# Performance work log

Measured on AMD Instinct MI355X. Metric: run time of the kernel, lower is better.

The kernel has to match this reference:

```python
import jax, jax.numpy as jnp
import numpy as np

PH, PW = 7, 7          # output_size
GRID = 2               # sampling_ratio
SCALES = (0.25, 0.125, 0.0625, 0.03125)  # 2^round(log2(feat/img)) per level
LVL_MIN, LVL_MAX = 2, 5                  # -log2(scales[0]), -log2(scales[-1])
CANON_SCALE, CANON_LVL = 224.0, 4.0
EPS = 1e-6


def setup_inputs() -> dict:
    key = jax.random.key(0)
    ks = jax.random.split(key, 6)
    B, C = 2, 256
    sizes = [(200, 200), (100, 100), (50, 50), (25, 25)]
    inp = {f"feat{i}": jax.random.normal(ks[i], (B, C, h, w), jnp.float32)
           for i, (h, w) in enumerate(sizes)}
    Nb = 256
    # boxes in 800x800 image coords, x1y1 + positive wh so 0<=x1<x2, 0<=y1<y2
    xy = jax.random.uniform(ks[4], (B, Nb, 2), jnp.float32, 0.0, 700.0)
    wh = jax.random.uniform(ks[5], (B, Nb, 2), jnp.float32, 32.0, 512.0)
    inp["boxes"] = jnp.concatenate([xy, xy + wh], axis=-1)
    return inp


def _roi_align_level(feat, b_idx, rois, scale):
    """torchvision roi_align, aligned=False. feat [B,C,H,W], rois [R,4] -> [R,C,PH,PW]."""
    H, W = feat.shape[2], feat.shape[3]
    x1 = rois[:, 0] * scale
    y1 = rois[:, 1] * scale
    x2 = rois[:, 2] * scale
    y2 = rois[:, 3] * scale
    roi_w = jnp.maximum(x2 - x1, 1.0)
    roi_h = jnp.maximum(y2 - y1, 1.0)
    bin_w = roi_w / PW
    bin_h = roi_h / PH
    # sub-bin sampling offsets: (bin + (i+0.5)/grid) for each bin, flattened [PH*GRID]
    gy = (jnp.arange(PH, dtype=jnp.float32)[:, None]
          + (jnp.arange(GRID, dtype=jnp.float32)[None, :] + 0.5) / GRID).reshape(-1)
    gx = (jnp.arange(PW, dtype=jnp.float32)[:, None]
          + (jnp.arange(GRID, dtype=jnp.float32)[None, :] + 0.5) / GRID).reshape(-1)
    ys = y1[:, None] + gy[None, :] * bin_h[:, None]   # [R, PH*G]
    xs = x1[:, None] + gx[None, :] * bin_w[:, None]   # [R, PW*G]
    y = ys[:, :, None]                                 # [R, PH*G, 1]
    x = xs[:, None, :]                                 # [R, 1, PW*G]
    valid = (y >= -1.0) & (y <= H) & (x >= -1.0) & (x <= W)
    yc = jnp.clip(y, 0.0, H - 1)
    xc = jnp.clip(x, 0.0, W - 1)
    yl = jnp.floor(yc).astype(jnp.int32)
    xl = jnp.floor(xc).astype(jnp.int32)
    yh = jnp.minimum(yl + 1, H - 1)
    xh = jnp.minimum(xl + 1, W - 1)
    ly = yc - yl.astype(yc.dtype)
    lx = xc - xl.astype(xc.dtype)
    hy = 1.0 - ly
    hx = 1.0 - lx
    b = b_idx[:, None, None]

    def gather(yi, xi):
        # advanced indexing with slice in channel dim -> [R, PH*G, PW*G, C]
        return feat[b, :, yi, xi]

    val = ((hy * hx)[..., None] * gather(yl, xl)
           + (hy * lx)[..., None] * gather(yl, xh)
           + (ly * hx)[..., None] * gather(yh, xl)
           + (ly * lx)[..., None] * gather(yh, xh))
    val = jnp.where(valid[..., None], val, 0.0)
    R, C = rois.shape[0], feat.shape[1]
    # average over the GRIDxGRID sampling points of each bin
    val = val.reshape(R, PH, GRID, PW, GRID, C).mean(axis=(2, 4))  # [R,PH,PW,C]
    return jnp.transpose(val, (0, 3, 1, 2))                        # [R,C,PH,PW]


def reference(feat0, feat1, feat2, feat3, boxes):
    feats = [feat0, feat1, feat2, feat3]
    B, Nb = boxes.shape[0], boxes.shape[1]
    rois = boxes.reshape(-1, 4)                               # convert_to_roi_format
    b_idx = jnp.repeat(jnp.arange(B), Nb)
    # LevelMapper (FPN eq. 1)
    s = jnp.sqrt(jnp.maximum((rois[:, 2] - rois[:, 0]) * (rois[:, 3] - rois[:, 1]), 0.0))
    lvl = jnp.floor(CANON_LVL + jnp.log2(s / CANON_SCALE + EPS))
    lvl = jnp.clip(lvl, LVL_MIN, LVL_MAX).astype(jnp.int32) - LVL_MIN  # [R] in [0,3]
    out = jnp.zeros((rois.shape[0], feats[0].shape[1], PH, PW), feats[0].dtype)
    for l, (f, sc) in enumerate(zip(feats, SCALES)):
        pooled = _roi_align_level(f, b_idx, rois, sc)
        out = jnp.where((lvl == l)[:, None, None, None], pooled, out)
    return out
```

## Files before the change

kernel.cpp:

```cpp
#include <hip/hip_runtime.h>


#define PHW 49
#define NCHUNK 8
#define CH 32
#define NC 4
#define PSIZE 1024

__global__ __launch_bounds__(256) void msroi_kernel(
    const float* __restrict__ f0, const float* __restrict__ f1,
    const float* __restrict__ f2, const float* __restrict__ f3,
    const float* __restrict__ boxes, float* __restrict__ out)
{
    const int C = 256, Nb = 256;
    const int r = blockIdx.x;
    const int chunk = blockIdx.y;
    const int tid = threadIdx.x;
    const int b = r / Nb;

    const float x1b = boxes[r * 4 + 0];
    const float y1b = boxes[r * 4 + 1];
    const float x2b = boxes[r * 4 + 2];
    const float y2b = boxes[r * 4 + 3];
    const float area = fmaxf((x2b - x1b) * (y2b - y1b), 0.0f);
    const float s = sqrtf(area);
    float lv = floorf(4.0f + log2f(s / 224.0f + 1e-6f));
    lv = fminf(fmaxf(lv, 2.0f), 5.0f);
    const int lvl = (int)lv - 2;

    const float* feat;
    int H, W;
    float scale;
    switch (lvl) {
        case 0:  feat = f0; H = 200; W = 200; scale = 0.25f;    break;
        case 1:  feat = f1; H = 100; W = 100; scale = 0.125f;   break;
        case 2:  feat = f2; H = 50;  W = 50;  scale = 0.0625f;  break;
        default: feat = f3; H = 25;  W = 25;  scale = 0.03125f; break;
    }
    const int HW = H * W;

    const float x1 = x1b * scale, y1 = y1b * scale;
    const float x2 = x2b * scale, y2 = y2b * scale;
    const float roi_w = fmaxf(x2 - x1, 1.0f);
    const float roi_h = fmaxf(y2 - y1, 1.0f);
    const float bin_w = roi_w * (1.0f / 7.0f);
    const float bin_h = roi_h * (1.0f / 7.0f);

    const float ys0 = fminf(fmaxf(y1 + 0.25f * bin_h, 0.0f), (float)(H - 1));
    const float ys1 = fminf(fmaxf(y1 + 6.75f * bin_h, 0.0f), (float)(H - 1));
    const float xs0 = fminf(fmaxf(x1 + 0.25f * bin_w, 0.0f), (float)(W - 1));
    const float xs1 = fminf(fmaxf(x1 + 6.75f * bin_w, 0.0f), (float)(W - 1));
    const int row0 = (int)floorf(ys0);
    const int row1 = min((int)floorf(ys1) + 1, H - 1);
    const int col0 = (int)floorf(xs0);
    const int col1 = min((int)floorf(xs1) + 1, W - 1);
    const int prows = row1 - row0 + 1;
    const int pcols = col1 - col0 + 1;
    const int psize = prows * pcols;
    const int wstride = W - pcols;
    const float inv_pcols = 1.0f / (float)pcols;

    int goff[4];
#pragma unroll
    for (int k = 0; k < 4; ++k) {
        const int e = tid + k * 256;
        const int ec = min(e, psize - 1);
        const int rr = (int)floorf(((float)ec + 0.5f) * inv_pcols);
        goff[k] = ec + rr * wstride;
    }

    const int bin = tid & 63;
    const bool active = bin < PHW;
    int   offs[16];
    float wts[16];
    {
        const int bb = active ? bin : 0;
        const int ph = bb / 7;
        const int pw = bb - ph * 7;
#pragma unroll
        for (int g = 0; g < 4; ++g) {
            const int iy = g >> 1, ix = g & 1;
            const float gy = (float)ph + ((float)iy + 0.5f) * 0.5f;
            const float gx = (float)pw + ((float)ix + 0.5f) * 0.5f;
            const float y = y1 + gy * bin_h;
            const float x = x1 + gx * bin_w;
            const bool valid = (y >= -1.0f) && (y <= (float)H) &&
                               (x >= -1.0f) && (x <= (float)W);
            const float yc = fminf(fmaxf(y, 0.0f), (float)(H - 1));
            const float xc = fminf(fmaxf(x, 0.0f), (float)(W - 1));
            const int yl = (int)floorf(yc);
            const int xl = (int)floorf(xc);
            const int yh = min(yl + 1, H - 1);
            const int xh = min(xl + 1, W - 1);
            const float ly = yc - (float)yl;
            const float lx = xc - (float)xl;
            const float hy = 1.0f - ly, hx = 1.0f - lx;
            const float m = valid ? 0.25f : 0.0f;
            const int ry0 = (yl - row0) * pcols, ry1 = (yh - row0) * pcols;
            const int cx0 = xl - col0, cx1 = xh - col0;
            offs[g * 4 + 0] = ry0 + cx0;  wts[g * 4 + 0] = hy * hx * m;
            offs[g * 4 + 1] = ry0 + cx1;  wts[g * 4 + 1] = hy * lx * m;
            offs[g * 4 + 2] = ry1 + cx0;  wts[g * 4 + 2] = ly * hx * m;
            offs[g * 4 + 3] = ry1 + cx1;  wts[g * 4 + 3] = ly * lx * m;
        }
    }

    __shared__ float lds[NC * PSIZE];
    const int cslot = tid >> 6;
    const int cbase = chunk * CH;
    const float* __restrict__ fch =
        feat + (size_t)(b * C + cbase) * HW + (row0 * W + col0);
    const size_t outBase = (size_t)r * C * PHW + (size_t)cbase * PHW;

    for (int cc = 0; cc < CH; cc += NC) {
        float buf[NC][4];
#pragma unroll
        for (int ch = 0; ch < NC; ++ch) {
            const float* __restrict__ gp = fch + (size_t)(cc + ch) * HW;
#pragma unroll
            for (int k = 0; k < 4; ++k)
                buf[ch][k] = gp[goff[k]];
        }
#pragma unroll
        for (int ch = 0; ch < NC; ++ch) {
#pragma unroll
            for (int k = 0; k < 4; ++k)
                lds[ch * PSIZE + tid + k * 256] = buf[ch][k];
        }
        __syncthreads();

        if (active) {
            const float* __restrict__ p = &lds[cslot * PSIZE];
            float acc = 0.0f;
#pragma unroll
            for (int k = 0; k < 16; ++k)
                acc += wts[k] * p[offs[k]];
            out[outBase + (size_t)(cc + cslot) * PHW + bin] = acc;
        }
        __syncthreads();
    }
}

extern "C" void kernel_launch(void* const* d_in, const int* in_sizes, int n_in,
                              void* d_out, int out_size, void* d_ws, size_t ws_size,
                              hipStream_t stream) {
    const float* f0 = (const float*)d_in[0];
    const float* f1 = (const float*)d_in[1];
    const float* f2 = (const float*)d_in[2];
    const float* f3 = (const float*)d_in[3];
    const float* boxes = (const float*)d_in[4];
    float* out = (float*)d_out;

    const int R = in_sizes[4] / 4;
    dim3 grid(R, NCHUNK);
    msroi_kernel<<<grid, 256, 0, stream>>>(f0, f1, f2, f3, boxes, out);
}
```

Baseline: 180.6 us.

## Use single-wave blocks with channel-interleaved float4 LDS and register prefetch

```diff
diff --git a/kernel.cpp b/kernel.cpp
--- a/kernel.cpp
+++ b/kernel.cpp
@@ -4,10 +4,9 @@
 #define PHW 49
 #define NCHUNK 8
 #define CH 32
-#define NC 4
 #define PSIZE 1024
 
-__global__ __launch_bounds__(256) void msroi_kernel(
+__global__ __launch_bounds__(64) void msroi_kernel(
     const float* __restrict__ f0, const float* __restrict__ f1,
     const float* __restrict__ f2, const float* __restrict__ f3,
     const float* __restrict__ boxes, float* __restrict__ out)
@@ -60,16 +59,17 @@
     const int wstride = W - pcols;
     const float inv_pcols = 1.0f / (float)pcols;
 
-    int goff[4];
+    int goff[16];
 #pragma unroll
-    for (int k = 0; k < 4; ++k) {
-        const int e = tid + k * 256;
+    for (int k = 0; k < 16; ++k) {
+        const int e = tid + k * 64;
         const int ec = min(e, psize - 1);
         const int rr = (int)floorf(((float)ec + 0.5f) * inv_pcols);
         goff[k] = ec + rr * wstride;
     }
+    const int kmax = (psize + 63) >> 6;
 
-    const int bin = tid & 63;
+    const int bin = tid;
     const bool active = bin < PHW;
     int   offs[16];
     float wts[16];
@@ -105,40 +105,60 @@
         }
     }
 
-    __shared__ float lds[NC * PSIZE];
-    const int cslot = tid >> 6;
+    __shared__ float4 lds4[PSIZE];
+
     const int cbase = chunk * CH;
     const float* __restrict__ fch =
         feat + (size_t)(b * C + cbase) * HW + (row0 * W + col0);
-    const size_t outBase = (size_t)r * C * PHW + (size_t)cbase * PHW;
+    float* __restrict__ outp =
+        out + (size_t)r * C * PHW + (size_t)cbase * PHW + bin;
 
-    for (int cc = 0; cc < CH; cc += NC) {
-        float buf[NC][4];
+    float4 buf[16];
+
+#define LOADR(CCV)                                                         \
+    do {                                                                   \
+        const float* __restrict__ g0 = fch + (size_t)((CCV) + 0) * HW;     \
+        const float* __restrict__ g1 = fch + (size_t)((CCV) + 1) * HW;     \
+        const float* __restrict__ g2 = fch + (size_t)((CCV) + 2) * HW;     \
+        const float* __restrict__ g3 = fch + (size_t)((CCV) + 3) * HW;     \
+        _Pragma("unroll")                                                  \
+        for (int k = 0; k < 16; ++k) {                                     \
+            if (k < kmax) {       \
+                buf[k].x = g0[goff[k]];                                    \
+                buf[k].y = g1[goff[k]];                                    \
+                buf[k].z = g2[goff[k]];                                    \
+                buf[k].w = g3[goff[k]];                                    \
+            }                                                              \
+        }                                                                  \
+    } while (0)
+
+    LOADR(0);
+    for (int cc = 0; cc < CH; cc += 4) {
+        __syncthreads();
 #pragma unroll
-        for (int ch = 0; ch < NC; ++ch) {
-            const float* __restrict__ gp = fch + (size_t)(cc + ch) * HW;
-#pragma unroll
-            for (int k = 0; k < 4; ++k)
-                buf[ch][k] = gp[goff[k]];
-        }
-#pragma unroll
-        for (int ch = 0; ch < NC; ++ch) {
-#pragma unroll
-            for (int k = 0; k < 4; ++k)
-                lds[ch * PSIZE + tid + k * 256] = buf[ch][k];
-        }
+        for (int k = 0; k < 16; ++k)
+            if (k < kmax) lds4[tid + k * 64] = buf[k];
         __syncthreads();
 
+        if (cc + 4 < CH) LOADR(cc + 4);
+
         if (active) {
-            const float* __restrict__ p = &lds[cslot * PSIZE];
-            float acc = 0.0f;
+            float4 acc = make_float4(0.0f, 0.0f, 0.0f, 0.0f);
 #pragma unroll
-            for (int k = 0; k < 16; ++k)
-                acc += wts[k] * p[offs[k]];
-            out[outBase + (size_t)(cc + cslot) * PHW + bin] = acc;
+            for (int j = 0; j < 16; ++j) {
+                const float4 v = lds4[offs[j]];
+                acc.x += wts[j] * v.x;
+                acc.y += wts[j] * v.y;
+                acc.z += wts[j] * v.z;
+                acc.w += wts[j] * v.w;
+            }
+            outp[(size_t)(cc + 0) * PHW] = acc.x;
+            outp[(size_t)(cc + 1) * PHW] = acc.y;
+            outp[(size_t)(cc + 2) * PHW] = acc.z;
+            outp[(size_t)(cc + 3) * PHW] = acc.w;
         }
-        __syncthreads();
     }
+#undef LOADR
 }
 
 extern "C" void kernel_launch(void* const* d_in, const int* in_sizes, int n_in,
@@ -153,5 +173,5 @@
 
     const int R = in_sizes[4] / 4;
     dim3 grid(R, NCHUNK);
-    msroi_kernel<<<grid, 256, 0, stream>>>(f0, f1, f2, f3, boxes, out);
+    msroi_kernel<<<grid, 64, 0, stream>>>(f0, f1, f2, f3, boxes, out);
 }
```

Measured after the change: 219.9 us. +21.8%, slower.

## Gather bilinear samples directly from global memory and remap workgroups across XCDs

Applied to the files above, without the earlier changes.

```diff
diff --git a/kernel.cpp b/kernel.cpp
--- a/kernel.cpp
+++ b/kernel.cpp
@@ -2,10 +2,6 @@
 
 
 #define PHW 49
-#define NCHUNK 8
-#define CH 32
-#define NC 4
-#define PSIZE 1024
 
 __global__ __launch_bounds__(256) void msroi_kernel(
     const float* __restrict__ f0, const float* __restrict__ f1,
@@ -13,9 +9,17 @@
     const float* __restrict__ boxes, float* __restrict__ out)
 {
     const int C = 256, Nb = 256;
-    const int r = blockIdx.x;
-    const int chunk = blockIdx.y;
+
+    const int nwg = gridDim.x;
+    const int cpx = nwg >> 3;
+    const int orig = blockIdx.x;
+    const int wgid = (orig & 7) * cpx + (orig >> 3);
+    const int r = wgid >> 2;
+    const int quarter = wgid & 3;
+
     const int tid = threadIdx.x;
+    const int w = tid >> 6;
+    const int lane = tid & 63;
     const int b = r / Nb;
 
     const float x1b = boxes[r * 4 + 0];
@@ -46,32 +50,9 @@
     const float bin_w = roi_w * (1.0f / 7.0f);
     const float bin_h = roi_h * (1.0f / 7.0f);
 
-    const float ys0 = fminf(fmaxf(y1 + 0.25f * bin_h, 0.0f), (float)(H - 1));
-    const float ys1 = fminf(fmaxf(y1 + 6.75f * bin_h, 0.0f), (float)(H - 1));
-    const float xs0 = fminf(fmaxf(x1 + 0.25f * bin_w, 0.0f), (float)(W - 1));
-    const float xs1 = fminf(fmaxf(x1 + 6.75f * bin_w, 0.0f), (float)(W - 1));
-    const int row0 = (int)floorf(ys0);
-    const int row1 = min((int)floorf(ys1) + 1, H - 1);
-    const int col0 = (int)floorf(xs0);
-    const int col1 = min((int)floorf(xs1) + 1, W - 1);
-    const int prows = row1 - row0 + 1;
-    const int pcols = col1 - col0 + 1;
-    const int psize = prows * pcols;
-    const int wstride = W - pcols;
-    const float inv_pcols = 1.0f / (float)pcols;
-
-    int goff[4];
-#pragma unroll
-    for (int k = 0; k < 4; ++k) {
-        const int e = tid + k * 256;
-        const int ec = min(e, psize - 1);
-        const int rr = (int)floorf(((float)ec + 0.5f) * inv_pcols);
-        goff[k] = ec + rr * wstride;
-    }
-
-    const int bin = tid & 63;
+    const int bin = lane;
     const bool active = bin < PHW;
-    int   offs[16];
+    int   goff[16];
     float wts[16];
     {
         const int bb = active ? bin : 0;
@@ -96,48 +77,28 @@
             const float lx = xc - (float)xl;
             const float hy = 1.0f - ly, hx = 1.0f - lx;
             const float m = valid ? 0.25f : 0.0f;
-            const int ry0 = (yl - row0) * pcols, ry1 = (yh - row0) * pcols;
-            const int cx0 = xl - col0, cx1 = xh - col0;
-            offs[g * 4 + 0] = ry0 + cx0;  wts[g * 4 + 0] = hy * hx * m;
-            offs[g * 4 + 1] = ry0 + cx1;  wts[g * 4 + 1] = hy * lx * m;
-            offs[g * 4 + 2] = ry1 + cx0;  wts[g * 4 + 2] = ly * hx * m;
-            offs[g * 4 + 3] = ry1 + cx1;  wts[g * 4 + 3] = ly * lx * m;
+            goff[g * 4 + 0] = yl * W + xl;  wts[g * 4 + 0] = hy * hx * m;
+            goff[g * 4 + 1] = yl * W + xh;  wts[g * 4 + 1] = hy * lx * m;
+            goff[g * 4 + 2] = yh * W + xl;  wts[g * 4 + 2] = ly * hx * m;
+            goff[g * 4 + 3] = yh * W + xh;  wts[g * 4 + 3] = ly * lx * m;
         }
     }
 
-    __shared__ float lds[NC * PSIZE];
-    const int cslot = tid >> 6;
-    const int cbase = chunk * CH;
-    const float* __restrict__ fch =
-        feat + (size_t)(b * C + cbase) * HW + (row0 * W + col0);
-    const size_t outBase = (size_t)r * C * PHW + (size_t)cbase * PHW;
+    const int c0 = quarter * 64 + w * 16;
+    const float* __restrict__ fpl = feat + (size_t)(b * C + c0) * HW;
+    float* __restrict__ op = out + (size_t)r * C * PHW
+                                 + (size_t)c0 * PHW + bin;
 
-    for (int cc = 0; cc < CH; cc += NC) {
-        float buf[NC][4];
-#pragma unroll
-        for (int ch = 0; ch < NC; ++ch) {
-            const float* __restrict__ gp = fch + (size_t)(cc + ch) * HW;
-#pragma unroll
-            for (int k = 0; k < 4; ++k)
-                buf[ch][k] = gp[goff[k]];
-        }
-#pragma unroll
-        for (int ch = 0; ch < NC; ++ch) {
-#pragma unroll
-            for (int k = 0; k < 4; ++k)
-                lds[ch * PSIZE + tid + k * 256] = buf[ch][k];
-        }
-        __syncthreads();
-
-        if (active) {
-            const float* __restrict__ p = &lds[cslot * PSIZE];
+    if (active) {
+#pragma unroll 2
+        for (int cc = 0; cc < 16; ++cc) {
+            const float* __restrict__ p = fpl + (size_t)cc * HW;
             float acc = 0.0f;
 #pragma unroll
-            for (int k = 0; k < 16; ++k)
-                acc += wts[k] * p[offs[k]];
-            out[outBase + (size_t)(cc + cslot) * PHW + bin] = acc;
+            for (int j = 0; j < 16; ++j)
+                acc += wts[j] * p[goff[j]];
+            op[(size_t)cc * PHW] = acc;
         }
-        __syncthreads();
     }
 }
 
@@ -152,6 +113,6 @@
     float* out = (float*)d_out;
 
     const int R = in_sizes[4] / 4;
-    dim3 grid(R, NCHUNK);
+    dim3 grid(R * 4);
     msroi_kernel<<<grid, 256, 0, stream>>>(f0, f1, f2, f3, boxes, out);
 }
```

Result: slower. 273.5 us (+51.4%).

## Double-buffer per-wave LDS patches via direct global-to-LDS loads, drop block barriers

Applied to the files above, without the earlier changes.

```diff
diff --git a/kernel.cpp b/kernel.cpp
--- a/kernel.cpp
+++ b/kernel.cpp
@@ -3,9 +3,8 @@
 
 #define PHW 49
 #define NCHUNK 8
-#define CH 32
-#define NC 4
-#define PSIZE 1024
+#define SLABN 896
+#define SMAXN 14
 
 __global__ __launch_bounds__(256) void msroi_kernel(
     const float* __restrict__ f0, const float* __restrict__ f1,
@@ -16,7 +15,12 @@
     const int r = blockIdx.x;
     const int chunk = blockIdx.y;
     const int tid = threadIdx.x;
+    const int w = tid >> 6;
+    const int lane = tid & 63;
     const int b = r / Nb;
+
+    const int bin = lane;
+    const bool active = bin < PHW;
 
     const float x1b = boxes[r * 4 + 0];
     const float y1b = boxes[r * 4 + 1];
@@ -60,19 +64,22 @@
     const int wstride = W - pcols;
     const float inv_pcols = 1.0f / (float)pcols;
 
-    int goff[4];
+    const int smax = (psize >> 6) + 1;
+    int gsrc[SMAXN];
 #pragma unroll
-    for (int k = 0; k < 4; ++k) {
-        const int e = tid + k * 256;
-        const int ec = min(e, psize - 1);
-        const int rr = (int)floorf(((float)ec + 0.5f) * inv_pcols);
-        goff[k] = ec + rr * wstride;
+    for (int k = 0; k < SMAXN; ++k) {
+        if (k < smax) {
+            const int e = k * 64 + lane;
+            const int ec = min(e, psize - 1);
+            const int rr = (int)floorf(((float)ec + 0.5f) * inv_pcols);
+            gsrc[k] = ec + rr * wstride;
+        } else {
+            gsrc[k] = 0;
+        }
     }
 
-    const int bin = tid & 63;
-    const bool active = bin < PHW;
-    int   offs[16];
-    float wts[16];
+    int   offs[8];
+    float wt0[8], wt1[8];
     {
         const int bb = active ? bin : 0;
         const int ph = bb / 7;
@@ -91,54 +98,64 @@
             const int yl = (int)floorf(yc);
             const int xl = (int)floorf(xc);
             const int yh = min(yl + 1, H - 1);
-            const int xh = min(xl + 1, W - 1);
             const float ly = yc - (float)yl;
             const float lx = xc - (float)xl;
             const float hy = 1.0f - ly, hx = 1.0f - lx;
             const float m = valid ? 0.25f : 0.0f;
-            const int ry0 = (yl - row0) * pcols, ry1 = (yh - row0) * pcols;
-            const int cx0 = xl - col0, cx1 = xh - col0;
-            offs[g * 4 + 0] = ry0 + cx0;  wts[g * 4 + 0] = hy * hx * m;
-            offs[g * 4 + 1] = ry0 + cx1;  wts[g * 4 + 1] = hy * lx * m;
-            offs[g * 4 + 2] = ry1 + cx0;  wts[g * 4 + 2] = ly * hx * m;
-            offs[g * 4 + 3] = ry1 + cx1;  wts[g * 4 + 3] = ly * lx * m;
+            const int cx0 = xl - col0;
+            offs[g * 2 + 0] = (yl - row0) * pcols + cx0;
+            wt0[g * 2 + 0] = hy * hx * m;
+            wt1[g * 2 + 0] = hy * lx * m;
+            offs[g * 2 + 1] = (yh - row0) * pcols + cx0;
+            wt0[g * 2 + 1] = ly * hx * m;
+            wt1[g * 2 + 1] = ly * lx * m;
         }
     }
 
-    __shared__ float lds[NC * PSIZE];
-    const int cslot = tid >> 6;
-    const int cbase = chunk * CH;
+    __shared__ float slabs[4][2][SLABN];
+
+    const int cw = chunk * 32 + w * 8;
     const float* __restrict__ fch =
-        feat + (size_t)(b * C + cbase) * HW + (row0 * W + col0);
-    const size_t outBase = (size_t)r * C * PHW + (size_t)cbase * PHW;
+        feat + (size_t)(b * C + cw) * HW + (row0 * W + col0);
+    float* __restrict__ op =
+        out + ((size_t)r * C + cw) * PHW + bin;
 
-    for (int cc = 0; cc < CH; cc += NC) {
-        float buf[NC][4];
+#define STAGE(BUF, CP)                                                     \
+    do {                                                                   \
+        const float* gp = fch + (size_t)(CP) * HW;                         \
+        _Pragma("unroll")                                                  \
+        for (int k = 0; k < SMAXN; ++k) {                                  \
+            if (k < smax) {                                                \
+                __builtin_amdgcn_global_load_lds(                          \
+                    (const __attribute__((address_space(1))) void*)        \
+                        (gp + gsrc[k]),                                    \
+                    (__attribute__((address_space(3))) void*)              \
+                        (&slabs[w][BUF][k * 64]),                          \
+                    4, 0, 0);                                              \
+            }                                                              \
+        }                                                                  \
+    } while (0)
+
+    STAGE(0, 0);
 #pragma unroll
-        for (int ch = 0; ch < NC; ++ch) {
-            const float* __restrict__ gp = fch + (size_t)(cc + ch) * HW;
-#pragma unroll
-            for (int k = 0; k < 4; ++k)
-                buf[ch][k] = gp[goff[k]];
-        }
-#pragma unroll
-        for (int ch = 0; ch < NC; ++ch) {
-#pragma unroll
-            for (int k = 0; k < 4; ++k)
-                lds[ch * PSIZE + tid + k * 256] = buf[ch][k];
-        }
-        __syncthreads();
-
+    for (int cp = 0; cp < 8; ++cp) {
+        asm volatile("s_waitcnt vmcnt(0)" ::: "memory");
+        __builtin_amdgcn_sched_barrier(0);
+        if (cp < 7) STAGE((cp + 1) & 1, cp + 1);
         if (active) {
-            const float* __restrict__ p = &lds[cslot * PSIZE];
+            const float* __restrict__ p = &slabs[w][cp & 1][0];
             float acc = 0.0f;
 #pragma unroll
-            for (int k = 0; k < 16; ++k)
-                acc += wts[k] * p[offs[k]];
-            out[outBase + (size_t)(cc + cslot) * PHW + bin] = acc;
+            for (int j = 0; j < 8; ++j) {
+                const float a0 = p[offs[j]];
+                const float a1 = p[offs[j] + 1];
+                acc = fmaf(wt0[j], a0, acc);
+                acc = fmaf(wt1[j], a1, acc);
+            }
+            op[(size_t)cp * PHW] = acc;
         }
-        __syncthreads();
     }
+#undef STAGE
 }
 
 extern "C" void kernel_launch(void* const* d_in, const int* in_sizes, int n_in,
```

New measurement: 178.8 us. About the same (-1.0%).
